# Performance work log

Measured on AMD Instinct MI355X. Metric: run time of the kernel, lower is better.

## Reference

```python
import jax, jax.numpy as jnp
import numpy as np
from math import exp

WINDOW_SIZE = 11
CHANNEL = 3
DATA_RANGE = 1.0
K1 = 0.01
K2 = 0.03


def _create_window(window_size=WINDOW_SIZE, channel=CHANNEL, sigma=1.5):
    g = np.array([exp(-(x - window_size // 2) ** 2 / float(2 * sigma ** 2))
                  for x in range(window_size)], dtype=np.float32)
    g = g / g.sum()
    w2d = np.outer(g, g).astype(np.float32)  # (k, k)
    # depthwise kernel, OIHW with I=1, O=channel
    return jnp.asarray(np.broadcast_to(w2d, (channel, 1, window_size, window_size)).copy())


def _depthwise_conv(x, window):
    pad = WINDOW_SIZE // 2
    return jax.lax.conv_general_dilated(
        x, window, window_strides=(1, 1),
        padding=[(pad, pad), (pad, pad)],
        dimension_numbers=('NCHW', 'OIHW', 'NCHW'),
        feature_group_count=CHANNEL)


def setup_inputs() -> dict:
    key = jax.random.key(0)
    k1, k2 = jax.random.split(key)
    img1 = jax.random.uniform(k1, (32, 3, 512, 512), dtype=jnp.float32)
    img2 = jax.random.uniform(k2, (32, 3, 512, 512), dtype=jnp.float32)
    return {"img1": img1, "img2": img2}


def reference(img1, img2):
    window = _create_window()
    mu1 = _depthwise_conv(img1, window)
    mu2 = _depthwise_conv(img2, window)
    mu1_sq = mu1 * mu1
    mu2_sq = mu2 * mu2
    mu1_mu2 = mu1 * mu2
    sigma1_sq = jnp.clip(_depthwise_conv(img1 * img1, window) - mu1_sq, 0.0, None)
    sigma2_sq = jnp.clip(_depthwise_conv(img2 * img2, window) - mu2_sq, 0.0, None)
    sigma12 = _depthwise_conv(img1 * img2, window) - mu1_mu2
    C1 = (K1 * DATA_RANGE) ** 2
    C2 = (K2 * DATA_RANGE) ** 2
    ssim_map = ((2 * mu1_mu2 + C1) * (2 * sigma12 + C2)) / ((mu1_sq + mu2_sq + C1) * (sigma1_sq + sigma2_sq + C2))
    return 1.0 - ssim_map.mean()
```

## Files before the change

kernel.cpp:

```cpp
#include <hip/hip_runtime.h>

#define W_IMG 512
#define H_IMG 512
#define PLANES 96
#define NPIX 25165824.0

#define SW 64
#define SH 64
#define NROWS (SH + 10)
#define NPAIR 38
#define WPB 4
#define XS (W_IMG / SW)
#define YB (H_IMG / SH)
#define BLOCKS_PER_PLANE (XS * YB / WPB)

__global__ void ssim_zero(double* acc) {
    if (threadIdx.x == 0) acc[0] = 0.0;
}

__global__ void ssim_final(const double* __restrict__ acc, float* __restrict__ out) {
    if (threadIdx.x == 0) out[0] = (float)(1.0 - acc[0] / NPIX);
}

__global__ __launch_bounds__(256, 2)
void ssim_main(const float* __restrict__ img1,
               const float* __restrict__ img2,
               double* __restrict__ acc)
{
    constexpr float G[11] = {
        0.00102838f, 0.00759875f, 0.03600077f, 0.10936070f, 0.21300540f,
        0.26601180f,
        0.21300540f, 0.10936070f, 0.03600077f, 0.00759875f, 0.00102838f };
    constexpr float C1 = 0.0001f;
    constexpr float C2 = 0.0009f;

    __shared__ __align__(16) float4 sbuf[WPB][2][NPAIR];
    __shared__ float wred[WPB];

    const int tid = threadIdx.x;
    const int wv  = tid >> 6;
    const int L   = tid & 63;
    const int wid = blockIdx.x * WPB + wv;
    const int c0  = (wid & (XS - 1)) * SW;
    const int r0  = (wid >> 3) * SH;
    const size_t pofs = (size_t)blockIdx.y * (H_IMG * W_IMG);
    const float* __restrict__ p1 = img1 + pofs;
    const float* __restrict__ p2 = img2 + pofs;

    const int p0  = (L + 1) >> 1;
    const bool odd = ((L + 1) & 1) == 0;

    float Gp[12];
    Gp[0] = odd ? 0.f : G[0];
    #pragma unroll
    for (int j = 1; j <= 10; ++j) Gp[j] = odd ? G[j - 1] : G[j];
    Gp[11] = odd ? G[10] : 0.f;

    const int gp = c0 - 6 + 2 * L;
    const bool sth = (L < NPAIR);
    const bool cok = sth && (gp >= 0) && (gp < W_IMG);

    float2 ra = make_float2(0.f, 0.f), rb = ra;
    auto LOADROW = [&](int s) {
        ra = make_float2(0.f, 0.f); rb = ra;
        const int gr = r0 - 5 + s;
        if (cok && (unsigned)gr < (unsigned)H_IMG) {
            const int off = gr * W_IMG + gp;
            ra = *(const float2*)(p1 + off);
            rb = *(const float2*)(p2 + off);
        }
    };

    float ring[5][11];
    float lsum = 0.f;

    LOADROW(0);
    if (sth) sbuf[wv][0][L] = make_float4(ra.x, rb.x, ra.y, rb.y);
    LOADROW(1);

    int cur = 0;
    #pragma unroll 1
    for (int sb = 0; sb < 77; sb += 11) {
        #pragma unroll
        for (int j = 0; j < 11; ++j) {
            const int s = sb + j;

            if (s + 1 < NROWS) {
                if (sth) sbuf[wv][cur ^ 1][L] = make_float4(ra.x, rb.x, ra.y, rb.y);
            }
            if (s + 2 < NROWS) LOADROW(s + 2);

            if (s < NROWS) {
                const float4 f0 = sbuf[wv][cur][p0 + 0];
                const float4 f1 = sbuf[wv][cur][p0 + 1];
                const float4 f2 = sbuf[wv][cur][p0 + 2];
                const float4 f3 = sbuf[wv][cur][p0 + 3];
                const float4 f4 = sbuf[wv][cur][p0 + 4];
                const float4 f5 = sbuf[wv][cur][p0 + 5];
                const float av[12] = { f0.x,f0.z, f1.x,f1.z, f2.x,f2.z,
                                       f3.x,f3.z, f4.x,f4.z, f5.x,f5.z };
                const float bv[12] = { f0.y,f0.w, f1.y,f1.w, f2.y,f2.w,
                                       f3.y,f3.w, f4.y,f4.w, f5.y,f5.w };
                float m1 = 0.f, m2 = 0.f, h11 = 0.f, h22 = 0.f, h12 = 0.f;
                #pragma unroll
                for (int q = 0; q < 12; ++q) {
                    const float t1 = Gp[q] * av[q];
                    const float t2 = Gp[q] * bv[q];
                    m1 += t1;  m2 += t2;
                    h11 = fmaf(t1, av[q], h11);
                    h22 = fmaf(t2, bv[q], h22);
                    h12 = fmaf(t1, bv[q], h12);
                }
                ring[0][j] = m1;  ring[1][j] = m2;
                ring[2][j] = h11; ring[3][j] = h22; ring[4][j] = h12;
            }

            if (s >= 10 && s < NROWS) {
                float M1 = 0.f, M2 = 0.f, E11 = 0.f, E22 = 0.f, E12 = 0.f;
                #pragma unroll
                for (int k = 0; k < 11; ++k) {
                    const int sl = (j + 1 + k) % 11;
                    M1  = fmaf(G[k], ring[0][sl], M1);
                    M2  = fmaf(G[k], ring[1][sl], M2);
                    E11 = fmaf(G[k], ring[2][sl], E11);
                    E22 = fmaf(G[k], ring[3][sl], E22);
                    E12 = fmaf(G[k], ring[4][sl], E12);
                }
                const float mu1s = M1 * M1, mu2s = M2 * M2, mu12 = M1 * M2;
                const float v11 = fmaxf(E11 - mu1s, 0.f);
                const float v22 = fmaxf(E22 - mu2s, 0.f);
                const float v12 = E12 - mu12;
                const float num = fmaf(2.f, mu12, C1) * fmaf(2.f, v12, C2);
                const float den = (mu1s + mu2s + C1) * (v11 + v22 + C2);
                lsum = fmaf(num, __builtin_amdgcn_rcpf(den), lsum);
            }

            cur ^= 1;
        }
    }

    #pragma unroll
    for (int off = 32; off > 0; off >>= 1)
        lsum += __shfl_down(lsum, off, 64);
    if (L == 0) wred[wv] = lsum;
    __syncthreads();
    if (tid == 0)
        atomicAdd(acc, (double)(wred[0] + wred[1] + wred[2] + wred[3]));
}

extern "C" void kernel_launch(void* const* d_in, const int* in_sizes, int n_in,
                              void* d_out, int out_size, void* d_ws, size_t ws_size,
                              hipStream_t stream) {
    const float* img1 = (const float*)d_in[0];
    const float* img2 = (const float*)d_in[1];
    float* out  = (float*)d_out;
    double* acc = (double*)d_ws;

    ssim_zero<<<dim3(1), dim3(64), 0, stream>>>(acc);
    ssim_main<<<dim3(BLOCKS_PER_PLANE, PLANES), dim3(256), 0, stream>>>(img1, img2, acc);
    ssim_final<<<dim3(1), dim3(64), 0, stream>>>(acc, out);
}
```

Measured before the change: 122.4 us.

## Drop LDS staging; load each row's window directly and use packed FP32 math

Each lane now reads its own 12-column horizontal window straight from global memory as three clamped, unaligned float4 loads per image. The shared-memory double buffer, its pair-interleaved layout and the odd/even Gaussian taps are removed, and per-lane coefficient masks zero out duplicated columns where the clamped loads overlap at the edges. The horizontal and vertical passes use v_pk_mul/add/fma_f32 inline assembly to process two values per instruction, and the vertical pass is reordered to run before the current row's ring slot is overwritten. This cuts LDS traffic and ALU instruction count but issues redundant overlapping global loads that depend on cache hits, and the inline assembly may limit compiler scheduling.

```diff
diff --git a/kernel.cpp b/kernel.cpp
--- a/kernel.cpp
+++ b/kernel.cpp
@@ -1,4 +1,6 @@
 #include <hip/hip_runtime.h>
+
+typedef float v2f __attribute__((ext_vector_type(2)));
 
 #define W_IMG 512
 #define H_IMG 512
@@ -8,7 +10,6 @@
 #define SW 64
 #define SH 64
 #define NROWS (SH + 10)
-#define NPAIR 38
 #define WPB 4
 #define XS (W_IMG / SW)
 #define YB (H_IMG / SH)
@@ -20,6 +21,22 @@
 
 __global__ void ssim_final(const double* __restrict__ acc, float* __restrict__ out) {
     if (threadIdx.x == 0) out[0] = (float)(1.0 - acc[0] / NPIX);
+}
+
+__device__ __forceinline__ float4 ld4u(const float* p) {
+    float4 v;
+    __builtin_memcpy(&v, p, 16);
+    return v;
+}
+
+__device__ __forceinline__ v2f pk_mul(v2f a, v2f b) {
+    v2f d; asm("v_pk_mul_f32 %0, %1, %2" : "=v"(d) : "v"(a), "v"(b)); return d;
+}
+__device__ __forceinline__ v2f pk_add(v2f a, v2f b) {
+    v2f d; asm("v_pk_add_f32 %0, %1, %2" : "=v"(d) : "v"(a), "v"(b)); return d;
+}
+__device__ __forceinline__ v2f pk_fma(v2f a, v2f b, v2f c) {
+    v2f d; asm("v_pk_fma_f32 %0, %1, %2, %3" : "=v"(d) : "v"(a), "v"(b), "v"(c)); return d;
 }
 
 __global__ __launch_bounds__(256, 2)
@@ -31,10 +48,9 @@
         0.00102838f, 0.00759875f, 0.03600077f, 0.10936070f, 0.21300540f,
         0.26601180f,
         0.21300540f, 0.10936070f, 0.03600077f, 0.00759875f, 0.00102838f };
-    constexpr float C1 = 0.0001f;
-    constexpr float C2 = 0.0009f;
-
-    __shared__ __align__(16) float4 sbuf[WPB][2][NPAIR];
+    constexpr float K_C1 = 0.0001f;
+    constexpr float K_C2 = 0.0009f;
+
     __shared__ float wred[WPB];
 
     const int tid = threadIdx.x;
@@ -47,95 +63,117 @@
     const float* __restrict__ p1 = img1 + pofs;
     const float* __restrict__ p2 = img2 + pofs;
 
-    const int p0  = (L + 1) >> 1;
-    const bool odd = ((L + 1) & 1) == 0;
-
-    float Gp[12];
-    Gp[0] = odd ? 0.f : G[0];
+    const int c  = c0 + L;
+    const int ws = c - 5;
+
+    int bofs[3];
     #pragma unroll
-    for (int j = 1; j <= 10; ++j) Gp[j] = odd ? G[j - 1] : G[j];
-    Gp[11] = odd ? G[10] : 0.f;
-
-    const int gp = c0 - 6 + 2 * L;
-    const bool sth = (L < NPAIR);
-    const bool cok = sth && (gp >= 0) && (gp < W_IMG);
-
-    float2 ra = make_float2(0.f, 0.f), rb = ra;
-    auto LOADROW = [&](int s) {
-        ra = make_float2(0.f, 0.f); rb = ra;
-        const int gr = r0 - 5 + s;
-        if (cok && (unsigned)gr < (unsigned)H_IMG) {
-            const int off = gr * W_IMG + gp;
-            ra = *(const float2*)(p1 + off);
-            rb = *(const float2*)(p2 + off);
+    for (int i = 0; i < 3; ++i) {
+        int bb = ws + 4 * i;
+        bb = bb < 0 ? 0 : bb;
+        bb = bb > (W_IMG - 4) ? (W_IMG - 4) : bb;
+        bofs[i] = bb;
+    }
+
+    float Cs[12];
+    {
+        int prev_end = -1;
+        #pragma unroll
+        for (int i = 0; i < 3; ++i) {
+            #pragma unroll
+            for (int jj = 0; jj < 4; ++jj) {
+                const int col = bofs[i] + jj;
+                const int tap = col - ws;
+                float g = 0.f;
+                #pragma unroll
+                for (int t = 0; t < 11; ++t) g = (tap == t) ? G[t] : g;
+                Cs[4 * i + jj] = (col > prev_end) ? g : 0.f;
+            }
+            prev_end = bofs[i] + 3;
         }
-    };
-
-    float ring[5][11];
+    }
+    v2f C2[6];
+    #pragma unroll
+    for (int p = 0; p < 6; ++p) { C2[p].x = Cs[2 * p]; C2[p].y = Cs[2 * p + 1]; }
+
+    v2f  ringA[11], ringB[11];
+    float ringC[11];
     float lsum = 0.f;
 
-    LOADROW(0);
-    if (sth) sbuf[wv][0][L] = make_float4(ra.x, rb.x, ra.y, rb.y);
-    LOADROW(1);
-
-    int cur = 0;
     #pragma unroll 1
     for (int sb = 0; sb < 77; sb += 11) {
         #pragma unroll
         for (int j = 0; j < 11; ++j) {
-            const int s = sb + j;
-
-            if (s + 1 < NROWS) {
-                if (sth) sbuf[wv][cur ^ 1][L] = make_float4(ra.x, rb.x, ra.y, rb.y);
-            }
-            if (s + 2 < NROWS) LOADROW(s + 2);
-
-            if (s < NROWS) {
-                const float4 f0 = sbuf[wv][cur][p0 + 0];
-                const float4 f1 = sbuf[wv][cur][p0 + 1];
-                const float4 f2 = sbuf[wv][cur][p0 + 2];
-                const float4 f3 = sbuf[wv][cur][p0 + 3];
-                const float4 f4 = sbuf[wv][cur][p0 + 4];
-                const float4 f5 = sbuf[wv][cur][p0 + 5];
-                const float av[12] = { f0.x,f0.z, f1.x,f1.z, f2.x,f2.z,
-                                       f3.x,f3.z, f4.x,f4.z, f5.x,f5.z };
-                const float bv[12] = { f0.y,f0.w, f1.y,f1.w, f2.y,f2.w,
-                                       f3.y,f3.w, f4.y,f4.w, f5.y,f5.w };
-                float m1 = 0.f, m2 = 0.f, h11 = 0.f, h22 = 0.f, h12 = 0.f;
-                #pragma unroll
-                for (int q = 0; q < 12; ++q) {
-                    const float t1 = Gp[q] * av[q];
-                    const float t2 = Gp[q] * bv[q];
-                    m1 += t1;  m2 += t2;
-                    h11 = fmaf(t1, av[q], h11);
-                    h22 = fmaf(t2, bv[q], h22);
-                    h12 = fmaf(t1, bv[q], h12);
-                }
-                ring[0][j] = m1;  ring[1][j] = m2;
-                ring[2][j] = h11; ring[3][j] = h22; ring[4][j] = h12;
-            }
-
-            if (s >= 10 && s < NROWS) {
-                float M1 = 0.f, M2 = 0.f, E11 = 0.f, E22 = 0.f, E12 = 0.f;
+            const int s  = sb + j;
+            const int gr = r0 - 5 + s;
+            const bool rv = (s < NROWS) && ((unsigned)gr < (unsigned)H_IMG);
+
+            float4 la0, la1, la2, lb0, lb1, lb2;
+            if (rv) {
+                const float* q1 = p1 + gr * W_IMG;
+                const float* q2 = p2 + gr * W_IMG;
+                la0 = ld4u(q1 + bofs[0]);
+                la1 = ld4u(q1 + bofs[1]);
+                la2 = ld4u(q1 + bofs[2]);
+                lb0 = ld4u(q2 + bofs[0]);
+                lb1 = ld4u(q2 + bofs[1]);
+                lb2 = ld4u(q2 + bofs[2]);
+            }
+
+            if (s >= 11 && s < SH + 11) {
+                v2f MA, MB;
+                MA.x = 0.f; MA.y = 0.f; MB.x = 0.f; MB.y = 0.f;
+                float e12 = 0.f;
                 #pragma unroll
                 for (int k = 0; k < 11; ++k) {
-                    const int sl = (j + 1 + k) % 11;
-                    M1  = fmaf(G[k], ring[0][sl], M1);
-                    M2  = fmaf(G[k], ring[1][sl], M2);
-                    E11 = fmaf(G[k], ring[2][sl], E11);
-                    E22 = fmaf(G[k], ring[3][sl], E22);
-                    E12 = fmaf(G[k], ring[4][sl], E12);
+                    const int sl = (j + k) % 11;
+                    v2f gg; gg.x = G[k]; gg.y = G[k];
+                    MA = pk_fma(gg, ringA[sl], MA);
+                    MB = pk_fma(gg, ringB[sl], MB);
+                    e12 = fmaf(G[k], ringC[sl], e12);
                 }
+                const float M1 = MA.x, M2 = MA.y, E11 = MB.x, E22 = MB.y;
                 const float mu1s = M1 * M1, mu2s = M2 * M2, mu12 = M1 * M2;
                 const float v11 = fmaxf(E11 - mu1s, 0.f);
                 const float v22 = fmaxf(E22 - mu2s, 0.f);
-                const float v12 = E12 - mu12;
-                const float num = fmaf(2.f, mu12, C1) * fmaf(2.f, v12, C2);
-                const float den = (mu1s + mu2s + C1) * (v11 + v22 + C2);
+                const float v12 = e12 - mu12;
+                const float num = fmaf(2.f, mu12, K_C1) * fmaf(2.f, v12, K_C2);
+                const float den = (mu1s + mu2s + K_C1) * (v11 + v22 + K_C2);
                 lsum = fmaf(num, __builtin_amdgcn_rcpf(den), lsum);
             }
 
-            cur ^= 1;
+            if (s < NROWS) {
+                if (rv) {
+                    v2f A[6], B[6];
+                    A[0].x = la0.x; A[0].y = la0.y;  A[1].x = la0.z; A[1].y = la0.w;
+                    A[2].x = la1.x; A[2].y = la1.y;  A[3].x = la1.z; A[3].y = la1.w;
+                    A[4].x = la2.x; A[4].y = la2.y;  A[5].x = la2.z; A[5].y = la2.w;
+                    B[0].x = lb0.x; B[0].y = lb0.y;  B[1].x = lb0.z; B[1].y = lb0.w;
+                    B[2].x = lb1.x; B[2].y = lb1.y;  B[3].x = lb1.z; B[3].y = lb1.w;
+                    B[4].x = lb2.x; B[4].y = lb2.y;  B[5].x = lb2.z; B[5].y = lb2.w;
+
+                    v2f m1v, m2v, h11v, h22v, h12v;
+                    m1v.x = 0.f; m1v.y = 0.f; m2v = m1v;
+                    h11v = m1v; h22v = m1v; h12v = m1v;
+                    #pragma unroll
+                    for (int p = 0; p < 6; ++p) {
+                        const v2f t1 = pk_mul(C2[p], A[p]);
+                        const v2f t2 = pk_mul(C2[p], B[p]);
+                        m1v  = pk_add(m1v, t1);
+                        m2v  = pk_add(m2v, t2);
+                        h11v = pk_fma(t1, A[p], h11v);
+                        h22v = pk_fma(t2, B[p], h22v);
+                        h12v = pk_fma(t1, B[p], h12v);
+                    }
+                    ringA[j].x = m1v.x + m1v.y;   ringA[j].y = m2v.x + m2v.y;
+                    ringB[j].x = h11v.x + h11v.y; ringB[j].y = h22v.x + h22v.y;
+                    ringC[j]   = h12v.x + h12v.y;
+                } else {
+                    ringA[j].x = 0.f; ringA[j].y = 0.f;
+                    ringB[j].x = 0.f; ringB[j].y = 0.f;
+                    ringC[j]   = 0.f;
+                }
+            }
         }
     }
 
```

New measurement: 123.8 us. Within noise of the previous version (+1.2%).

## Compute two columns per lane with packed FP32 math and fused variance terms

Applied to the files above, without the earlier changes.

Each lane now produces two adjacent output columns. Strips widen to 128 columns and blocks shrink to two waves. The horizontal and vertical Gaussian passes use v_pk_fma/v_pk_mul packed FP32 instructions. The separate a², b² accumulators are replaced by a single (a+b)² term, and sigma1²+sigma2² is recovered as E[(a+b)²]-2E[ab]. Global loads become 16-byte quads and the block-level atomic is split into per-plane double accumulators reduced by the final kernel. These changes cut ALU instruction count and atomic contention, at the cost of higher register pressure from the 44-entry packed ring, a slight numerical change from the algebraic identity, and fewer waves per block.

```diff
diff --git a/kernel.cpp b/kernel.cpp
--- a/kernel.cpp
+++ b/kernel.cpp
@@ -1,82 +1,101 @@
 #include <hip/hip_runtime.h>
+
+typedef float v2f __attribute__((ext_vector_type(2)));
 
 #define W_IMG 512
 #define H_IMG 512
 #define PLANES 96
 #define NPIX 25165824.0
 
-#define SW 64
+#define SWIDE 128
 #define SH 64
 #define NROWS (SH + 10)
-#define NPAIR 38
-#define WPB 4
-#define XS (W_IMG / SW)
+#define NQUAD 36
+#define NPRS  72
+#define XS (W_IMG / SWIDE)
 #define YB (H_IMG / SH)
-#define BLOCKS_PER_PLANE (XS * YB / WPB)
+#define WPB 2
 
 __global__ void ssim_zero(double* acc) {
-    if (threadIdx.x == 0) acc[0] = 0.0;
+    const int t = threadIdx.x;
+    if (t < PLANES) acc[t] = 0.0;
 }
 
 __global__ void ssim_final(const double* __restrict__ acc, float* __restrict__ out) {
-    if (threadIdx.x == 0) out[0] = (float)(1.0 - acc[0] / NPIX);
+    const int L = threadIdx.x;
+    double s = (L < PLANES) ? acc[L] : 0.0;
+    if (L + 64 < PLANES) s += acc[L + 64];
+    #pragma unroll
+    for (int off = 32; off > 0; off >>= 1) s += __shfl_down(s, off, 64);
+    if (L == 0) out[0] = (float)(1.0 - s / NPIX);
 }
 
-__global__ __launch_bounds__(256, 2)
+__device__ __forceinline__ v2f pk_add2(v2f a, v2f b) {
+    v2f d; asm("v_pk_add_f32 %0, %1, %2" : "=v"(d) : "v"(a), "v"(b)); return d;
+}
+__device__ __forceinline__ v2f pk_mul2(v2f a, v2f b) {
+    v2f d; asm("v_pk_mul_f32 %0, %1, %2" : "=v"(d) : "v"(a), "v"(b)); return d;
+}
+__device__ __forceinline__ v2f pk_fma2(v2f a, v2f b, v2f c) {
+    asm("v_pk_fma_f32 %0, %1, %2, %0" : "+v"(c) : "v"(a), "v"(b)); return c;
+}
+
+__global__ __launch_bounds__(128, 2)
 void ssim_main(const float* __restrict__ img1,
                const float* __restrict__ img2,
                double* __restrict__ acc)
 {
-    constexpr float G[11] = {
-        0.00102838f, 0.00759875f, 0.03600077f, 0.10936070f, 0.21300540f,
-        0.26601180f,
-        0.21300540f, 0.10936070f, 0.03600077f, 0.00759875f, 0.00102838f };
-    constexpr float C1 = 0.0001f;
-    constexpr float C2 = 0.0009f;
+    constexpr float G0=0.00102838f, G1=0.00759875f, G2c=0.03600077f,
+                    G3=0.10936070f, G4=0.21300540f, G5=0.26601180f,
+                    G6=0.21300540f, G7=0.10936070f, G8=0.03600077f,
+                    G9=0.00759875f, G10=0.00102838f;
+    constexpr float K_C1 = 0.0001f;
+    constexpr float K_C2 = 0.0009f;
 
-    __shared__ __align__(16) float4 sbuf[WPB][2][NPAIR];
-    __shared__ float wred[WPB];
+    const v2f Gp1[6] = { {0.f,G0}, {G1,G2c}, {G3,G4}, {G5,G6}, {G7,G8}, {G9,G10} };
+    const v2f Gp2[6] = { {G0,G1}, {G2c,G3}, {G4,G5}, {G6,G7}, {G8,G9}, {G10,0.f} };
+    const v2f GV[11] = { {G0,G0},{G1,G1},{G2c,G2c},{G3,G3},{G4,G4},{G5,G5},
+                         {G6,G6},{G7,G7},{G8,G8},{G9,G9},{G10,G10} };
+
+    __shared__ __align__(16) float4 sp[WPB][2][NPRS];
 
     const int tid = threadIdx.x;
     const int wv  = tid >> 6;
     const int L   = tid & 63;
     const int wid = blockIdx.x * WPB + wv;
-    const int c0  = (wid & (XS - 1)) * SW;
-    const int r0  = (wid >> 3) * SH;
-    const size_t pofs = (size_t)blockIdx.y * (H_IMG * W_IMG);
+    const int c0  = (wid & (XS - 1)) * SWIDE;
+    const int r0  = (wid >> 2) * SH;
+    const int plane = blockIdx.y;
+    const size_t pofs = (size_t)plane * (H_IMG * W_IMG);
     const float* __restrict__ p1 = img1 + pofs;
     const float* __restrict__ p2 = img2 + pofs;
 
-    const int p0  = (L + 1) >> 1;
-    const bool odd = ((L + 1) & 1) == 0;
+    const int gq  = c0 - 8 + 4 * L;
+    const bool qok = (L < NQUAD) && (gq >= 0) && (gq <= W_IMG - 4);
+    const bool sth = (L < NQUAD);
 
-    float Gp[12];
-    Gp[0] = odd ? 0.f : G[0];
-    #pragma unroll
-    for (int j = 1; j <= 10; ++j) Gp[j] = odd ? G[j - 1] : G[j];
-    Gp[11] = odd ? G[10] : 0.f;
-
-    const int gp = c0 - 6 + 2 * L;
-    const bool sth = (L < NPAIR);
-    const bool cok = sth && (gp >= 0) && (gp < W_IMG);
-
-    float2 ra = make_float2(0.f, 0.f), rb = ra;
+    float4 qa = make_float4(0.f,0.f,0.f,0.f), qb = qa;
     auto LOADROW = [&](int s) {
-        ra = make_float2(0.f, 0.f); rb = ra;
+        qa = make_float4(0.f,0.f,0.f,0.f); qb = qa;
         const int gr = r0 - 5 + s;
-        if (cok && (unsigned)gr < (unsigned)H_IMG) {
-            const int off = gr * W_IMG + gp;
-            ra = *(const float2*)(p1 + off);
-            rb = *(const float2*)(p2 + off);
+        if (qok && (unsigned)gr < (unsigned)H_IMG) {
+            const int off = gr * W_IMG + gq;
+            __builtin_memcpy(&qa, p1 + off, 16);
+            __builtin_memcpy(&qb, p2 + off, 16);
+        }
+    };
+    auto STORE = [&](int buf) {
+        if (sth) {
+            sp[wv][buf][2*L]   = make_float4(qa.x, qa.y, qb.x, qb.y);
+            sp[wv][buf][2*L+1] = make_float4(qa.z, qa.w, qb.z, qb.w);
         }
     };
 
-    float ring[5][11];
+    v2f ring_m1[11], ring_m2[11], ring_ab[11], ring_s2[11];
     float lsum = 0.f;
+    const v2f z2 = {0.f, 0.f};
 
-    LOADROW(0);
-    if (sth) sbuf[wv][0][L] = make_float4(ra.x, rb.x, ra.y, rb.y);
-    LOADROW(1);
+    LOADROW(0); STORE(0); LOADROW(1);
 
     int cur = 0;
     #pragma unroll 1
@@ -85,54 +104,67 @@
         for (int j = 0; j < 11; ++j) {
             const int s = sb + j;
 
-            if (s + 1 < NROWS) {
-                if (sth) sbuf[wv][cur ^ 1][L] = make_float4(ra.x, rb.x, ra.y, rb.y);
-            }
+            if (s + 1 < NROWS) STORE(cur ^ 1);
             if (s + 2 < NROWS) LOADROW(s + 2);
 
             if (s < NROWS) {
-                const float4 f0 = sbuf[wv][cur][p0 + 0];
-                const float4 f1 = sbuf[wv][cur][p0 + 1];
-                const float4 f2 = sbuf[wv][cur][p0 + 2];
-                const float4 f3 = sbuf[wv][cur][p0 + 3];
-                const float4 f4 = sbuf[wv][cur][p0 + 4];
-                const float4 f5 = sbuf[wv][cur][p0 + 5];
-                const float av[12] = { f0.x,f0.z, f1.x,f1.z, f2.x,f2.z,
-                                       f3.x,f3.z, f4.x,f4.z, f5.x,f5.z };
-                const float bv[12] = { f0.y,f0.w, f1.y,f1.w, f2.y,f2.w,
-                                       f3.y,f3.w, f4.y,f4.w, f5.y,f5.w };
-                float m1 = 0.f, m2 = 0.f, h11 = 0.f, h22 = 0.f, h12 = 0.f;
+                v2f m1a=z2, m2a=z2, aba=z2, s2a=z2;
+                v2f m1b=z2, m2b=z2, abb=z2, s2b=z2;
                 #pragma unroll
-                for (int q = 0; q < 12; ++q) {
-                    const float t1 = Gp[q] * av[q];
-                    const float t2 = Gp[q] * bv[q];
-                    m1 += t1;  m2 += t2;
-                    h11 = fmaf(t1, av[q], h11);
-                    h22 = fmaf(t2, bv[q], h22);
-                    h12 = fmaf(t1, bv[q], h12);
+                for (int p = 0; p < 7; ++p) {
+                    const float4 P = sp[wv][cur][L + 1 + p];
+                    const v2f ap = {P.x, P.y};
+                    const v2f bp = {P.z, P.w};
+                    const v2f spp = pk_add2(ap, bp);
+                    if (p < 6) {
+                        const v2f g = Gp1[p];
+                        m1a = pk_fma2(g, ap, m1a);
+                        m2a = pk_fma2(g, bp, m2a);
+                        const v2f t1 = pk_mul2(g, ap);
+                        aba = pk_fma2(t1, bp, aba);
+                        const v2f t2 = pk_mul2(g, spp);
+                        s2a = pk_fma2(t2, spp, s2a);
+                    }
+                    if (p > 0) {
+                        const v2f g = Gp2[p - 1];
+                        m1b = pk_fma2(g, ap, m1b);
+                        m2b = pk_fma2(g, bp, m2b);
+                        const v2f t1 = pk_mul2(g, ap);
+                        abb = pk_fma2(t1, bp, abb);
+                        const v2f t2 = pk_mul2(g, spp);
+                        s2b = pk_fma2(t2, spp, s2b);
+                    }
                 }
-                ring[0][j] = m1;  ring[1][j] = m2;
-                ring[2][j] = h11; ring[3][j] = h22; ring[4][j] = h12;
+                ring_m1[j] = (v2f){ m1a.x + m1a.y, m1b.x + m1b.y };
+                ring_m2[j] = (v2f){ m2a.x + m2a.y, m2b.x + m2b.y };
+                ring_ab[j] = (v2f){ aba.x + aba.y, abb.x + abb.y };
+                ring_s2[j] = (v2f){ s2a.x + s2a.y, s2b.x + s2b.y };
             }
 
             if (s >= 10 && s < NROWS) {
-                float M1 = 0.f, M2 = 0.f, E11 = 0.f, E22 = 0.f, E12 = 0.f;
+                v2f M1=z2, M2=z2, AB=z2, S2=z2;
                 #pragma unroll
                 for (int k = 0; k < 11; ++k) {
                     const int sl = (j + 1 + k) % 11;
-                    M1  = fmaf(G[k], ring[0][sl], M1);
-                    M2  = fmaf(G[k], ring[1][sl], M2);
-                    E11 = fmaf(G[k], ring[2][sl], E11);
-                    E22 = fmaf(G[k], ring[3][sl], E22);
-                    E12 = fmaf(G[k], ring[4][sl], E12);
+                    M1 = pk_fma2(GV[k], ring_m1[sl], M1);
+                    M2 = pk_fma2(GV[k], ring_m2[sl], M2);
+                    AB = pk_fma2(GV[k], ring_ab[sl], AB);
+                    S2 = pk_fma2(GV[k], ring_s2[sl], S2);
                 }
-                const float mu1s = M1 * M1, mu2s = M2 * M2, mu12 = M1 * M2;
-                const float v11 = fmaxf(E11 - mu1s, 0.f);
-                const float v22 = fmaxf(E22 - mu2s, 0.f);
-                const float v12 = E12 - mu12;
-                const float num = fmaf(2.f, mu12, C1) * fmaf(2.f, v12, C2);
-                const float den = (mu1s + mu2s + C1) * (v11 + v22 + C2);
-                lsum = fmaf(num, __builtin_amdgcn_rcpf(den), lsum);
+                #pragma unroll
+                for (int h = 0; h < 2; ++h) {
+                    const float u1 = h ? M1.y : M1.x;
+                    const float u2 = h ? M2.y : M2.x;
+                    const float eab = h ? AB.y : AB.x;
+                    const float es2 = h ? S2.y : S2.x;
+                    const float mu12 = u1 * u2;
+                    const float musq = fmaf(u1, u1, u2 * u2);
+                    const float sig12 = eab - mu12;
+                    const float sigsum = fmaxf(fmaf(-2.f, eab, es2) - musq, 0.f);
+                    const float num = fmaf(2.f, mu12, K_C1) * fmaf(2.f, sig12, K_C2);
+                    const float den = (musq + K_C1) * (sigsum + K_C2);
+                    lsum = fmaf(num, __builtin_amdgcn_rcpf(den), lsum);
+                }
             }
 
             cur ^= 1;
@@ -142,10 +174,8 @@
     #pragma unroll
     for (int off = 32; off > 0; off >>= 1)
         lsum += __shfl_down(lsum, off, 64);
-    if (L == 0) wred[wv] = lsum;
-    __syncthreads();
-    if (tid == 0)
-        atomicAdd(acc, (double)(wred[0] + wred[1] + wred[2] + wred[3]));
+    if (L == 0)
+        atomicAdd(&acc[plane], (double)lsum);
 }
 
 extern "C" void kernel_launch(void* const* d_in, const int* in_sizes, int n_in,
@@ -156,7 +186,7 @@
     float* out  = (float*)d_out;
     double* acc = (double*)d_ws;
 
-    ssim_zero<<<dim3(1), dim3(64), 0, stream>>>(acc);
-    ssim_main<<<dim3(BLOCKS_PER_PLANE, PLANES), dim3(256), 0, stream>>>(img1, img2, acc);
+    ssim_zero<<<dim3(1), dim3(128), 0, stream>>>(acc);
+    ssim_main<<<dim3(XS * YB / WPB, PLANES), dim3(64 * WPB), 0, stream>>>(img1, img2, acc);
     ssim_final<<<dim3(1), dim3(64), 0, stream>>>(acc, out);
 }
```

After: 115.7 us. 1.06x faster.
